# Optimization experiments

Hardware: AMD Instinct MI355X
Metric: run time of the kernel (lower is better)

Reference implementation:

```python
import jax, jax.numpy as jnp
import numpy as np

BS, C, N, D = 4, 4, 2048, 16
K = 32    # k_size
M = 64    # kernel_num


def setup_inputs() -> dict:
    key = jax.random.key(0)
    ks = jax.random.split(key, 6)
    pos = jax.random.normal(ks[0], (BS, C, N, 3), jnp.float32)
    node_fea = jax.random.normal(ks[1], (BS, C, N, D), jnp.float32)
    node_mask = jnp.ones((BS, N), jnp.float32)
    angle_weight = jax.random.uniform(ks[2], (M, K * C), jnp.float32, -1.0, 1.0)
    scalar_weight = jax.random.uniform(ks[3], (2 * C * D, M), jnp.float32, 0.0, 1.0)
    radius_weight_1 = jax.random.uniform(ks[4], (1, M), jnp.float32, -1.0, 1.0)
    radius_weight_2 = jax.random.uniform(ks[5], (M, 1), jnp.float32, -1.0, 1.0)
    return dict(pos=pos, node_fea=node_fea, node_mask=node_mask,
                angle_weight=angle_weight, scalar_weight=scalar_weight,
                radius_weight_1=radius_weight_1, radius_weight_2=radius_weight_2)


def _gather_neighbors(t, idx):
    # t: (bs,c,n,dim), idx: (bs,c,n,k) -> (bs,c,n,k,dim)
    return jnp.take_along_axis(t[:, :, None, :, :], idx[:, :, :, :, None], axis=3)


def _forward(pos, node_fea, node_mask, angle_weight, scalar_weight,
             radius_weight_1, radius_weight_2):
    bs, c, n, _ = pos.shape
    m = angle_weight.shape[0]
    k = angle_weight.shape[1] // c
    d = node_fea.shape[-1]

    # ---- kNN graph from squared pairwise distances (get_edge) ----
    inner = jnp.einsum('bcnd,bcmd->bcnm', pos, pos)
    quad = jnp.sum(pos * pos, axis=-1)                              # (bs,c,n)
    dist = -2.0 * inner + quad[:, :, None, :] + quad[:, :, :, None]  # (bs,c,n,n)
    neg_vals, idx = jax.lax.top_k(-dist, k + 1)                      # k+1 smallest
    distances = -neg_vals[..., 1:]                                   # drop self, (bs,c,n,k)
    edge_index = idx[..., 1:]

    # ---- angular features (cos_theta) ----
    pos_ngb = _gather_neighbors(pos, edge_index)                     # (bs,c,n,k,3)
    dirs = pos_ngb - pos[:, :, :, None, :]
    nrm = jnp.maximum(jnp.linalg.norm(dirs, axis=-1, keepdims=True), 1e-12)
    dirs = dirs / nrm
    nearest = dirs[:, :, :, 0, :]                                    # (bs,c,n,3)
    cos_else = jnp.einsum('bcnkd,bcnd->bcnk', dirs[:, :, :, 1:, :], nearest)
    cos0 = jnp.concatenate([jnp.ones_like(cos_else[..., :1]), cos_else], axis=-1)
    theta = cos0 * node_mask[:, None, :, None]                       # (bs,c,n,k)
    theta = jnp.transpose(theta, (0, 2, 3, 1))                       # (bs,n,k,c)
    fea_struct = jnp.einsum('mf,bnf->bmn', angle_weight,
                            theta.reshape(bs, n, k * c))             # (bs,m,n)

    # ---- feature fusion ----
    fea_neigh = _gather_neighbors(node_fea, edge_index)              # (bs,c,n,k,d)
    node_rep = jnp.broadcast_to(node_fea[:, :, :, None, :], fea_neigh.shape)
    fea_cat = jnp.concatenate([node_rep, fea_neigh], axis=-1)        # (bs,c,n,k,2d)
    fea_cat = jnp.transpose(fea_cat, (0, 2, 3, 1, 4))                # (bs,n,k,c,2d)
    fea_cat = fea_cat * node_mask[:, :, None, None, None]

    # ---- distance-based message gating ----
    a = jax.nn.relu(distances[..., None] * radius_weight_1[0])       # (bs,c,n,k,m)
    b = jax.nn.relu(jnp.einsum('bcnkm,mo->bcnko', a, radius_weight_2))[..., 0]
    g = b * node_mask[:, None, :, None]                              # (bs,c,n,k)
    gate = jax.nn.sigmoid(jnp.transpose(g, (0, 2, 3, 1)))            # (bs,n,k,c)

    # ---- gated elementwise fusion + combination ----
    fea_gated = (gate[..., None] * fea_cat).reshape(bs, n, k, c * 2 * d)
    fea_elem = jnp.einsum('bnkf,fm->bnm', fea_gated, scalar_weight)  # sum over k
    interactions = jax.nn.leaky_relu(
        jnp.transpose(fea_elem, (0, 2, 1)) + fea_struct, 0.01)       # (bs,m,n)
    return interactions * node_mask[:, None, :]


def reference(pos, node_fea, node_mask, angle_weight, scalar_weight,
              radius_weight_1, radius_weight_2):
    return _forward(pos, node_fea, node_mask, angle_weight, scalar_weight,
                    radius_weight_1, radius_weight_2)
```

## Files before the change

kernel.cpp:

```cpp
#include <hip/hip_runtime.h>
#include <math.h>

#define BS 4
#define C 4
#define N 2048
#define D 16
#define KNN 32
#define M 64

typedef unsigned long long u64;
typedef unsigned int u32;
typedef unsigned short u16;


__device__ __forceinline__ u32 umin_u32(u32 a, u32 b) { return a < b ? a : b; }

#define DPP_MIN_STAGE(v, ctrl)                                                  \
    v = umin_u32(v, (u32)__builtin_amdgcn_update_dpp(                           \
                        (int)0xFFFFFFFF, (int)(v), (ctrl), 0xF, 0xF, false))

__device__ __forceinline__ u32 wave_min_dpp(u32 v) {
    DPP_MIN_STAGE(v, 0x111);
    DPP_MIN_STAGE(v, 0x112);
    DPP_MIN_STAGE(v, 0x114);
    DPP_MIN_STAGE(v, 0x118);
    DPP_MIN_STAGE(v, 0x142);
    DPP_MIN_STAGE(v, 0x143);
    return (u32)__builtin_amdgcn_readlane((int)v, 63);
}

#define DPP_ADD_STAGE(v, ctrl)                                                  \
    v += __int_as_float(__builtin_amdgcn_update_dpp(                            \
        0, __float_as_int(v), (ctrl), 0xF, 0xF, false))

__device__ __forceinline__ float wave_sum_dpp(float v) {
    DPP_ADD_STAGE(v, 0x111);
    DPP_ADD_STAGE(v, 0x112);
    DPP_ADD_STAGE(v, 0x114);
    DPP_ADD_STAGE(v, 0x118);
    DPP_ADD_STAGE(v, 0x142);
    DPP_ADD_STAGE(v, 0x143);
    return __int_as_float(__builtin_amdgcn_readlane(__float_as_int(v), 63));
}

__device__ __forceinline__ u32 mbcnt64(u64 m) {
    return __builtin_amdgcn_mbcnt_hi((u32)(m >> 32),
                                     __builtin_amdgcn_mbcnt_lo((u32)m, 0));
}

__device__ __forceinline__ float np_quad(float x, float y, float z) {
#pragma clang fp contract(off)
    float q = (x * x + y * y) + z * z;
    return q;
}

__device__ __forceinline__ float np_s(const float4& m2, const float4& p) {
#pragma clang fp contract(off)
    float t = (m2.x * p.x + m2.y * p.y) + m2.z * p.z;
    float s = t + p.w;
    return s;
}

__device__ __forceinline__ float np_dist2(const float4& m2, const float4& p) {
#pragma clang fp contract(off)
    float dist = np_s(m2, p) + m2.w;
    return dist;
}

__device__ __forceinline__ float4 fold_m2(const float4& me) {
    return make_float4(-2.0f * me.x, -2.0f * me.y, -2.0f * me.z, me.w);
}

__device__ __forceinline__ u32 flip_bits(float dist) {
    u32 b = __float_as_uint(dist);
    return b ^ (0x80000000u | (u32)((int)b >> 31));
}

__device__ __forceinline__ u64 dist_key(float dist, int j) {
    return ((u64)flip_bits(dist) << 32) | (u32)j;
}

__device__ __forceinline__ void emit_rank(u64* sl, int cnt, int row, int lane,
                                          u16* __restrict__ edge_ws,
                                          float* __restrict__ dist_ws) {
    if (lane < 4) sl[cnt + lane] = ~0ull;
    u64 own1 = sl[lane];
    if (lane >= cnt) own1 = ~0ull;
    int r1 = 0;
    for (int i = 0; i < cnt; i += 4) {
        u64 s0 = sl[i], s1 = sl[i + 1], s2 = sl[i + 2], s3 = sl[i + 3];
        r1 += (s0 < own1) + (s1 < own1) + (s2 < own1) + (s3 < own1);
    }
    if (r1 >= 1 && r1 <= KNN) {
        u32 fk = (u32)(own1 >> 32);
        u32 bb = (fk & 0x80000000u) ? (fk ^ 0x80000000u) : ~fk;
        edge_ws[(size_t)row * KNN + r1 - 1] = (u16)(u32)own1;
        dist_ws[(size_t)row * KNN + r1 - 1] = __uint_as_float(bb);
    }
    if (cnt > 64) {
        u64 own2 = (64 + lane < cnt) ? sl[64 + lane] : ~0ull;
        int r2 = 0;
        for (int i = 0; i < cnt; i += 4) {
            u64 s0 = sl[i], s1 = sl[i + 1], s2 = sl[i + 2], s3 = sl[i + 3];
            r2 += (s0 < own2) + (s1 < own2) + (s2 < own2) + (s3 < own2);
        }
        if (r2 >= 1 && r2 <= KNN) {
            u32 fk = (u32)(own2 >> 32);
            u32 bb = (fk & 0x80000000u) ? (fk ^ 0x80000000u) : ~fk;
            edge_ws[(size_t)row * KNN + r2 - 1] = (u16)(u32)own2;
            dist_ws[(size_t)row * KNN + r2 - 1] = __uint_as_float(bb);
        }
    }
}

__device__ __attribute__((noinline)) void slow_row(const float4* sp, float4 m2,
                                                   int row, int lane,
                                                   u16* __restrict__ edge_ws,
                                                   float* __restrict__ dist_ws) {
    u64 thr = 0ull;
    for (int s = 0; s <= KNN; ++s) {
        u64 best = ~0ull;
        for (int jj = 0; jj < 32; ++jj) {
            int j = jj * 64 + lane;
            u64 x = dist_key(np_dist2(m2, sp[j]), j);
            if (x > thr && x < best) best = x;
        }
        u32 bh = (u32)(best >> 32);
        u32 rh = wave_min_dpp(bh);
        u32 bl = (bh == rh) ? (u32)best : 0xFFFFFFFFu;
        u32 rl = wave_min_dpp(bl);
        thr = ((u64)rh << 32) | rl;
        if (s >= 1 && lane == s - 1) {
            u32 bb = (rh & 0x80000000u) ? (rh ^ 0x80000000u) : ~rh;
            edge_ws[(size_t)row * KNN + s - 1] = (u16)rl;
            dist_ws[(size_t)row * KNN + s - 1] = __uint_as_float(bb);
        }
    }
}

__device__ __forceinline__ void compact_emit(const float4* sp, int n, float pd,
                                             u64* sl, int row, int lane,
                                             u16* __restrict__ edge_ws,
                                             float* __restrict__ dist_ws) {
    float4 m2 = fold_m2(sp[n]);
    u32 base = 0;
#pragma unroll 2
    for (int jj = 0; jj < 32; ++jj) {
        int j = jj * 64 + lane;
        float d = np_dist2(m2, sp[j]);
        bool s = d <= pd;
        u64 m = __ballot(s);
        u32 pos = base + mbcnt64(m);
        if (s && pos < 128) sl[pos] = ((u64)flip_bits(d) << 32) | (u32)j;
        base += (u32)__popcll(m);
    }
    if ((int)base <= 124) emit_rank(sl, (int)base, row, lane, edge_ws, dist_ws);
    else                  slow_row(sp, m2, row, lane, edge_ws, dist_ws);
}

__global__ __launch_bounds__(512, 6) void knn_kernel(const float* __restrict__ pos,
                                                     u16* __restrict__ edge_ws,
                                                     float* __restrict__ dist_ws,
                                                     const float* __restrict__ aw,
                                                     const float* __restrict__ sw,
                                                     float* __restrict__ aw4,
                                                     float* __restrict__ sw4) {
    __shared__ float4 sp[N];
    __shared__ u64 slots[8][128];
    const int tid  = threadIdx.x;
    const int lane = tid & 63;
    const int wave = tid >> 6;
    const int rb   = blockIdx.x * 32;
    const int bc   = rb >> 11;

    const float* posr = pos + (size_t)bc * (N * 3);
    for (int j = tid; j < N; j += 512) {
        float x = posr[3 * j], y = posr[3 * j + 1], z = posr[3 * j + 2];
        sp[j] = make_float4(x, y, z, np_quad(x, y, z));
    }

    if (blockIdx.x == 0) {
#pragma unroll
        for (int it = 0; it < 16; ++it) {
            int i = it * 512 + tid;
            int f = i >> 6, mm = i & 63;
            int idx = (f >> 2) * 256 + mm * 4 + (f & 3);
            aw4[idx] = aw[mm * 128 + f];
            sw4[idx] = sw[i];
        }
    }
    __syncthreads();

    const int rowA = rb + wave * 4;
    const int nA   = rowA & (N - 1);
    const float4 m2A = fold_m2(sp[nA]);
    const float4 m2B = fold_m2(sp[nA + 1]);
    const float4 m2C = fold_m2(sp[nA + 2]);
    const float4 m2D = fold_m2(sp[nA + 3]);

    float mnA = __builtin_inff(), mnB = __builtin_inff();
    float mnC = __builtin_inff(), mnD = __builtin_inff();
#pragma unroll 4
    for (int jj = 0; jj < 32; ++jj) {
        int j = jj * 64 + lane;
        float4 p = sp[j];
        mnA = fminf(mnA, np_s(m2A, p));
        mnB = fminf(mnB, np_s(m2B, p));
        mnC = fminf(mnC, np_s(m2C, p));
        mnD = fminf(mnD, np_s(m2D, p));
    }

    float vA = mnA, vB = mnB, vC = mnC, vD = mnD;
#pragma unroll
    for (int k = 2; k <= 64; k <<= 1) {
#pragma unroll
        for (int j = k >> 1; j > 0; j >>= 1) {
            bool keepmin = (((lane & k) == 0) == ((lane & j) == 0));
            float oA = __int_as_float(__shfl_xor(__float_as_int(vA), j));
            float oB = __int_as_float(__shfl_xor(__float_as_int(vB), j));
            float oC = __int_as_float(__shfl_xor(__float_as_int(vC), j));
            float oD = __int_as_float(__shfl_xor(__float_as_int(vD), j));
            vA = ((oA < vA) == keepmin) ? oA : vA;
            vB = ((oB < vB) == keepmin) ? oB : vB;
            vC = ((oC < vC) == keepmin) ? oC : vC;
            vD = ((oD < vD) == keepmin) ? oD : vD;
        }
    }
    float pdA, pdB, pdC, pdD;
    {
#pragma clang fp contract(off)
        pdA = __int_as_float(__builtin_amdgcn_readlane(__float_as_int(vA), 32)) + m2A.w;
        pdB = __int_as_float(__builtin_amdgcn_readlane(__float_as_int(vB), 32)) + m2B.w;
        pdC = __int_as_float(__builtin_amdgcn_readlane(__float_as_int(vC), 32)) + m2C.w;
        pdD = __int_as_float(__builtin_amdgcn_readlane(__float_as_int(vD), 32)) + m2D.w;
    }

    compact_emit(sp, nA,     pdA, slots[wave], rowA,     lane, edge_ws, dist_ws);
    compact_emit(sp, nA + 1, pdB, slots[wave], rowA + 1, lane, edge_ws, dist_ws);
    compact_emit(sp, nA + 2, pdC, slots[wave], rowA + 2, lane, edge_ws, dist_ws);
    compact_emit(sp, nA + 3, pdD, slots[wave], rowA + 3, lane, edge_ws, dist_ws);
}

__global__ __launch_bounds__(512) void conv_kernel(
    const float* __restrict__ pos, const float* __restrict__ node_fea,
    const float* __restrict__ node_mask, const float* __restrict__ aw4,
    const float* __restrict__ sw4, const float* __restrict__ w1,
    const float* __restrict__ w2, const u16* __restrict__ edge_ws,
    const float* __restrict__ dist_ws, float* __restrict__ out) {
    __shared__ __align__(16) float theta_lds[8][128];
    __shared__ float gate_lds[8][128];
    __shared__ u16   edge_lds[8][128];
    __shared__ __align__(16) float h_lds[8][128];
    __shared__ float gsum_lds[8][4];
    __shared__ float outv[8][65];

    const int tid  = threadIdx.x;
    const int lane = tid & 63;
    const int wave = tid >> 6;

    const int row0 = blockIdx.x * 8;
    const int b    = row0 >> 11;
    const int n0   = row0 & (N - 1);
    const int row  = row0 + wave;
    const int n    = row & (N - 1);
    const float mval = node_mask[b * N + n];

    float S = wave_sum_dpp(fmaxf(w1[lane], 0.f) * w2[lane]);

#pragma unroll
    for (int it = 0; it < 2; ++it) {
        int p  = it * 64 + lane;
        int cc = p >> 5, kk = p & 31;
        int rowc = (b * C + cc) * N + n;
        int e      = edge_ws[(size_t)rowc * KNN + kk];
        float dist = dist_ws[(size_t)rowc * KNN + kk];
        const float* pp = pos + (size_t)rowc * 3;
        const float* qp = pos + ((size_t)(b * C + cc) * N + e) * 3;
        float dx = qp[0] - pp[0], dy = qp[1] - pp[1], dz = qp[2] - pp[2];
        float nrm = fmaxf(sqrtf(dx * dx + dy * dy + dz * dz), 1e-12f);
        float inv = 1.0f / nrm;
        dx *= inv; dy *= inv; dz *= inv;
        int src = lane & 32;
        float n0x = __shfl(dx, src), n0y = __shfl(dy, src), n0z = __shfl(dz, src);
        float cosv = (kk == 0) ? 1.f : (dx * n0x + dy * n0y + dz * n0z);
        theta_lds[wave][kk * 4 + cc] = cosv * mval;

        float g = fmaxf(dist * S, 0.f) * mval;
        float gate = 1.f / (1.f + expf(-g));
        gate_lds[wave][cc * 32 + kk] = gate;
        edge_lds[wave][cc * 32 + kk] = (u16)e;
        float gs = gate;
#pragma unroll
        for (int off = 1; off < 32; off <<= 1) gs += __shfl_xor(gs, off);
        if (kk == 0) gsum_lds[wave][cc] = gs;
    }

    {
        int cc = lane >> 4, dd = lane & 15;
        const float* nf = node_fea + (size_t)(b * C + cc) * N * D;
        float own = nf[(size_t)n * D + dd];
        h_lds[wave][cc * 32 + dd] = own * mval * gsum_lds[wave][cc];
        float acc = 0.f;
#pragma unroll
        for (int k = 0; k < 32; ++k) {
            int e = edge_lds[wave][cc * 32 + k];
            acc += gate_lds[wave][cc * 32 + k] * nf[(size_t)e * D + dd];
        }
        h_lds[wave][cc * 32 + 16 + dd] = acc * mval;
    }

    {
        const float4* wa4 = (const float4*)aw4;
        const float4* wv4 = (const float4*)sw4;
        const float4* th4 = (const float4*)(&theta_lds[wave][0]);
        const float4* hh4 = (const float4*)(&h_lds[wave][0]);
        float fs = 0.f, fe = 0.f;
#pragma unroll 4
        for (int f4 = 0; f4 < 32; ++f4) {
            float4 wa = wa4[f4 * 64 + lane];
            float4 wv = wv4[f4 * 64 + lane];
            float4 tv = th4[f4];
            float4 hv = hh4[f4];
            fs += wa.x * tv.x + wa.y * tv.y + wa.z * tv.z + wa.w * tv.w;
            fe += wv.x * hv.x + wv.y * hv.y + wv.z * hv.z + wv.w * hv.w;
        }
        float v = fs + fe;
        v = (v > 0.f) ? v : 0.01f * v;
        outv[wave][lane] = v * mval;
    }
    __syncthreads();

    {
        int m = tid >> 3, j = tid & 7;
        out[((size_t)(b * 64 + m)) * N + n0 + j] = outv[j][m];
    }
}

extern "C" void kernel_launch(void* const* d_in, const int* in_sizes, int n_in,
                              void* d_out, int out_size, void* d_ws, size_t ws_size,
                              hipStream_t stream) {
    const float* pos       = (const float*)d_in[0];
    const float* node_fea  = (const float*)d_in[1];
    const float* node_mask = (const float*)d_in[2];
    const float* aw        = (const float*)d_in[3];
    const float* sw        = (const float*)d_in[4];
    const float* w1        = (const float*)d_in[5];
    const float* w2        = (const float*)d_in[6];
    float* out = (float*)d_out;

    float* dist_ws = (float*)d_ws;
    u16*   edge_ws = (u16*)((char*)d_ws + 4u * 1024 * 1024);
    float* aw4     = (float*)((char*)d_ws + 6u * 1024 * 1024);
    float* sw4     = (float*)((char*)d_ws + 6u * 1024 * 1024 + 32u * 1024);

    knn_kernel<<<BS * C * N / 32, 512, 0, stream>>>(pos, edge_ws, dist_ws,
                                                    aw, sw, aw4, sw4);
    conv_kernel<<<BS * N / 8, 512, 0, stream>>>(pos, node_fea, node_mask, aw4, sw4,
                                                w1, w2, edge_ws, dist_ws, out);
}
```

Measured before the change: 153.6 us.

## Use SoA shared positions and packed f32 math in kNN distance scans

Changes the shared-memory point cloud from float4 AoS to four SoA arrays and computes two candidate distances per lane per iteration using v_pk_mul_f32/v_pk_add_f32 inline asm. Each lane now handles adjacent pairs of points rather than a 64-strided pattern, which halves the VALU instruction count for the distance math and allows 64-bit LDS loads. The aim is to reduce ALU and LDS-instruction cost in the min-scan and compaction passes. The compaction order changes (pairs of points per lane), and the packed ops must keep the non-contracted rounding to stay bit-exact with the reference.

```diff
diff --git a/kernel.cpp b/kernel.cpp
--- a/kernel.cpp
+++ b/kernel.cpp
@@ -11,7 +11,19 @@
 typedef unsigned long long u64;
 typedef unsigned int u32;
 typedef unsigned short u16;
-
+typedef float f32x2 __attribute__((ext_vector_type(2)));
+
+
+__device__ __forceinline__ f32x2 pk_mul(f32x2 a, f32x2 b) {
+    f32x2 d;
+    asm("v_pk_mul_f32 %0, %1, %2" : "=v"(d) : "v"(a), "v"(b));
+    return d;
+}
+__device__ __forceinline__ f32x2 pk_add(f32x2 a, f32x2 b) {
+    f32x2 d;
+    asm("v_pk_add_f32 %0, %1, %2" : "=v"(d) : "v"(a), "v"(b));
+    return d;
+}
 
 __device__ __forceinline__ u32 umin_u32(u32 a, u32 b) { return a < b ? a : b; }
 
@@ -54,30 +66,37 @@
     return q;
 }
 
-__device__ __forceinline__ float np_s(const float4& m2, const float4& p) {
+struct Q2 { f32x2 x, y, z, w; };
+
+__device__ __forceinline__ Q2 make_q2(float x, float y, float z, float q) {
+    Q2 r;
+    float mx = -2.0f * x, my = -2.0f * y, mz = -2.0f * z;
+    r.x.x = mx; r.x.y = mx;
+    r.y.x = my; r.y.y = my;
+    r.z.x = mz; r.z.y = mz;
+    r.w.x = q;  r.w.y = q;
+    return r;
+}
+
+__device__ __forceinline__ f32x2 np_s2(const Q2& q, f32x2 px, f32x2 py,
+                                       f32x2 pz, f32x2 pw) {
+    return pk_add(pk_add(pk_add(pk_mul(q.x, px), pk_mul(q.y, py)),
+                         pk_mul(q.z, pz)),
+                  pw);
+}
+
+__device__ __forceinline__ float np_dist_s(float m2x, float m2y, float m2z,
+                                           float qw, float px, float py,
+                                           float pz, float pw) {
 #pragma clang fp contract(off)
-    float t = (m2.x * p.x + m2.y * p.y) + m2.z * p.z;
-    float s = t + p.w;
-    return s;
-}
-
-__device__ __forceinline__ float np_dist2(const float4& m2, const float4& p) {
-#pragma clang fp contract(off)
-    float dist = np_s(m2, p) + m2.w;
+    float t = (m2x * px + m2y * py) + m2z * pz;
+    float dist = (t + pw) + qw;
     return dist;
-}
-
-__device__ __forceinline__ float4 fold_m2(const float4& me) {
-    return make_float4(-2.0f * me.x, -2.0f * me.y, -2.0f * me.z, me.w);
 }
 
 __device__ __forceinline__ u32 flip_bits(float dist) {
     u32 b = __float_as_uint(dist);
     return b ^ (0x80000000u | (u32)((int)b >> 31));
-}
-
-__device__ __forceinline__ u64 dist_key(float dist, int j) {
-    return ((u64)flip_bits(dist) << 32) | (u32)j;
 }
 
 __device__ __forceinline__ void emit_rank(u64* sl, int cnt, int row, int lane,
@@ -113,16 +132,17 @@
     }
 }
 
-__device__ __attribute__((noinline)) void slow_row(const float4* sp, float4 m2,
-                                                   int row, int lane,
-                                                   u16* __restrict__ edge_ws,
-                                                   float* __restrict__ dist_ws) {
+__device__ __attribute__((noinline)) void slow_row(
+    const float* spx, const float* spy, const float* spz, const float* spw,
+    float m2x, float m2y, float m2z, float qw, int row, int lane,
+    u16* __restrict__ edge_ws, float* __restrict__ dist_ws) {
     u64 thr = 0ull;
     for (int s = 0; s <= KNN; ++s) {
         u64 best = ~0ull;
         for (int jj = 0; jj < 32; ++jj) {
             int j = jj * 64 + lane;
-            u64 x = dist_key(np_dist2(m2, sp[j]), j);
+            float d = np_dist_s(m2x, m2y, m2z, qw, spx[j], spy[j], spz[j], spw[j]);
+            u64 x = ((u64)flip_bits(d) << 32) | (u32)j;
             if (x > thr && x < best) best = x;
         }
         u32 bh = (u32)(best >> 32);
@@ -138,24 +158,39 @@
     }
 }
 
-__device__ __forceinline__ void compact_emit(const float4* sp, int n, float pd,
-                                             u64* sl, int row, int lane,
-                                             u16* __restrict__ edge_ws,
-                                             float* __restrict__ dist_ws) {
-    float4 m2 = fold_m2(sp[n]);
+__device__ __forceinline__ void compact_emit(
+    const float* spx, const float* spy, const float* spz, const float* spw,
+    int n, float pd, u64* sl, int row, int lane,
+    u16* __restrict__ edge_ws, float* __restrict__ dist_ws) {
+    Q2 q = make_q2(spx[n], spy[n], spz[n], spw[n]);
     u32 base = 0;
-#pragma unroll 2
-    for (int jj = 0; jj < 32; ++jj) {
-        int j = jj * 64 + lane;
-        float d = np_dist2(m2, sp[j]);
-        bool s = d <= pd;
-        u64 m = __ballot(s);
-        u32 pos = base + mbcnt64(m);
-        if (s && pos < 128) sl[pos] = ((u64)flip_bits(d) << 32) | (u32)j;
-        base += (u32)__popcll(m);
+    const int lb = lane * 2;
+#pragma unroll 4
+    for (int t = 0; t < 16; ++t) {
+        int e0 = t * 128 + lb;
+        f32x2 px = *(const f32x2*)&spx[e0];
+        f32x2 py = *(const f32x2*)&spy[e0];
+        f32x2 pz = *(const f32x2*)&spz[e0];
+        f32x2 pw = *(const f32x2*)&spw[e0];
+        f32x2 d  = pk_add(np_s2(q, px, py, pz, pw), q.w);
+        {
+            bool s = d.x <= pd;
+            u64 m = __ballot(s);
+            u32 pos = base + mbcnt64(m);
+            if (s && pos < 128) sl[pos] = ((u64)flip_bits(d.x) << 32) | (u32)e0;
+            base += (u32)__popcll(m);
+        }
+        {
+            bool s = d.y <= pd;
+            u64 m = __ballot(s);
+            u32 pos = base + mbcnt64(m);
+            if (s && pos < 128) sl[pos] = ((u64)flip_bits(d.y) << 32) | (u32)(e0 + 1);
+            base += (u32)__popcll(m);
+        }
     }
     if ((int)base <= 124) emit_rank(sl, (int)base, row, lane, edge_ws, dist_ws);
-    else                  slow_row(sp, m2, row, lane, edge_ws, dist_ws);
+    else slow_row(spx, spy, spz, spw, q.x.x, q.y.x, q.z.x, q.w.x, row, lane,
+                  edge_ws, dist_ws);
 }
 
 __global__ __launch_bounds__(512, 6) void knn_kernel(const float* __restrict__ pos,
@@ -165,7 +200,10 @@
                                                      const float* __restrict__ sw,
                                                      float* __restrict__ aw4,
                                                      float* __restrict__ sw4) {
-    __shared__ float4 sp[N];
+    __shared__ __align__(16) float spx[N];
+    __shared__ __align__(16) float spy[N];
+    __shared__ __align__(16) float spz[N];
+    __shared__ __align__(16) float spw[N];
     __shared__ u64 slots[8][128];
     const int tid  = threadIdx.x;
     const int lane = tid & 63;
@@ -176,7 +214,7 @@
     const float* posr = pos + (size_t)bc * (N * 3);
     for (int j = tid; j < N; j += 512) {
         float x = posr[3 * j], y = posr[3 * j + 1], z = posr[3 * j + 2];
-        sp[j] = make_float4(x, y, z, np_quad(x, y, z));
+        spx[j] = x; spy[j] = y; spz[j] = z; spw[j] = np_quad(x, y, z);
     }
 
     if (blockIdx.x == 0) {
@@ -193,24 +231,36 @@
 
     const int rowA = rb + wave * 4;
     const int nA   = rowA & (N - 1);
-    const float4 m2A = fold_m2(sp[nA]);
-    const float4 m2B = fold_m2(sp[nA + 1]);
-    const float4 m2C = fold_m2(sp[nA + 2]);
-    const float4 m2D = fold_m2(sp[nA + 3]);
-
-    float mnA = __builtin_inff(), mnB = __builtin_inff();
-    float mnC = __builtin_inff(), mnD = __builtin_inff();
-#pragma unroll 4
-    for (int jj = 0; jj < 32; ++jj) {
-        int j = jj * 64 + lane;
-        float4 p = sp[j];
-        mnA = fminf(mnA, np_s(m2A, p));
-        mnB = fminf(mnB, np_s(m2B, p));
-        mnC = fminf(mnC, np_s(m2C, p));
-        mnD = fminf(mnD, np_s(m2D, p));
-    }
-
-    float vA = mnA, vB = mnB, vC = mnC, vD = mnD;
+    const Q2 qA = make_q2(spx[nA],     spy[nA],     spz[nA],     spw[nA]);
+    const Q2 qB = make_q2(spx[nA + 1], spy[nA + 1], spz[nA + 1], spw[nA + 1]);
+    const Q2 qC = make_q2(spx[nA + 2], spy[nA + 2], spz[nA + 2], spw[nA + 2]);
+    const Q2 qD = make_q2(spx[nA + 3], spy[nA + 3], spz[nA + 3], spw[nA + 3]);
+
+    f32x2 mnA, mnB, mnC, mnD;
+    mnA.x = mnA.y = __builtin_inff();
+    mnB.x = mnB.y = __builtin_inff();
+    mnC.x = mnC.y = __builtin_inff();
+    mnD.x = mnD.y = __builtin_inff();
+    const int lb = lane * 2;
+#pragma unroll
+    for (int t = 0; t < 16; ++t) {
+        int e0 = t * 128 + lb;
+        f32x2 px = *(const f32x2*)&spx[e0];
+        f32x2 py = *(const f32x2*)&spy[e0];
+        f32x2 pz = *(const f32x2*)&spz[e0];
+        f32x2 pw = *(const f32x2*)&spw[e0];
+        f32x2 sA = np_s2(qA, px, py, pz, pw);
+        f32x2 sB = np_s2(qB, px, py, pz, pw);
+        f32x2 sC = np_s2(qC, px, py, pz, pw);
+        f32x2 sD = np_s2(qD, px, py, pz, pw);
+        mnA.x = fminf(mnA.x, sA.x); mnA.y = fminf(mnA.y, sA.y);
+        mnB.x = fminf(mnB.x, sB.x); mnB.y = fminf(mnB.y, sB.y);
+        mnC.x = fminf(mnC.x, sC.x); mnC.y = fminf(mnC.y, sC.y);
+        mnD.x = fminf(mnD.x, sD.x); mnD.y = fminf(mnD.y, sD.y);
+    }
+
+    float vA = fminf(mnA.x, mnA.y), vB = fminf(mnB.x, mnB.y);
+    float vC = fminf(mnC.x, mnC.y), vD = fminf(mnD.x, mnD.y);
 #pragma unroll
     for (int k = 2; k <= 64; k <<= 1) {
 #pragma unroll
@@ -229,16 +279,16 @@
     float pdA, pdB, pdC, pdD;
     {
 #pragma clang fp contract(off)
-        pdA = __int_as_float(__builtin_amdgcn_readlane(__float_as_int(vA), 32)) + m2A.w;
-        pdB = __int_as_float(__builtin_amdgcn_readlane(__float_as_int(vB), 32)) + m2B.w;
-        pdC = __int_as_float(__builtin_amdgcn_readlane(__float_as_int(vC), 32)) + m2C.w;
-        pdD = __int_as_float(__builtin_amdgcn_readlane(__float_as_int(vD), 32)) + m2D.w;
-    }
-
-    compact_emit(sp, nA,     pdA, slots[wave], rowA,     lane, edge_ws, dist_ws);
-    compact_emit(sp, nA + 1, pdB, slots[wave], rowA + 1, lane, edge_ws, dist_ws);
-    compact_emit(sp, nA + 2, pdC, slots[wave], rowA + 2, lane, edge_ws, dist_ws);
-    compact_emit(sp, nA + 3, pdD, slots[wave], rowA + 3, lane, edge_ws, dist_ws);
+        pdA = __int_as_float(__builtin_amdgcn_readlane(__float_as_int(vA), 32)) + qA.w.x;
+        pdB = __int_as_float(__builtin_amdgcn_readlane(__float_as_int(vB), 32)) + qB.w.x;
+        pdC = __int_as_float(__builtin_amdgcn_readlane(__float_as_int(vC), 32)) + qC.w.x;
+        pdD = __int_as_float(__builtin_amdgcn_readlane(__float_as_int(vD), 32)) + qD.w.x;
+    }
+
+    compact_emit(spx, spy, spz, spw, nA,     pdA, slots[wave], rowA,     lane, edge_ws, dist_ws);
+    compact_emit(spx, spy, spz, spw, nA + 1, pdB, slots[wave], rowA + 1, lane, edge_ws, dist_ws);
+    compact_emit(spx, spy, spz, spw, nA + 2, pdC, slots[wave], rowA + 2, lane, edge_ws, dist_ws);
+    compact_emit(spx, spy, spz, spw, nA + 3, pdD, slots[wave], rowA + 3, lane, edge_ws, dist_ws);
 }
 
 __global__ __launch_bounds__(512) void conv_kernel(
```

Result: slower. 190.0 us (+23.8%).
